# Performance work log

Hardware: AMD Instinct MI355X
Metric: run time of the kernel (lower is better)

Reference implementation:

```python
import jax, jax.numpy as jnp
import numpy as np
import math

N_HEAD = 16
HEAD_QKV = 1024  # total qkv width; head_dim = HEAD_QKV // N_HEAD
WM_DECAY_LENGTH = 2048
WM_DECAY_RATE = 1.0
WM_ECHOIC = 16


def decay_weight_matrix(n):
    # power_law decay, faithful to get_decay_weight_matrix
    dl = WM_DECAY_LENGTH - WM_ECHOIC + 1
    nums = jnp.linspace(0.0, 1.0, dl)
    decay_values = 1.0 - jnp.power(nums, 1.0 / (np.e * WM_DECAY_RATE))
    decay_values = jnp.concatenate([jnp.ones(WM_ECHOIC - 1), decay_values])  # [WM_DECAY_LENGTH]
    decay_values = decay_values[:n]
    idx = jnp.arange(n)[:, None] - jnp.arange(n)[None, :]  # [n,n], negative above diag
    mat = decay_values[jnp.clip(idx, 0, n - 1)]
    return jnp.tril(mat).astype(jnp.float32)


def setup_inputs() -> dict:
    key = jax.random.key(0)
    k1, k2, k3 = jax.random.split(key, 3)
    B, T, C = 2, 2048, 1024
    x = jax.random.normal(k1, (B, T, C), dtype=jnp.float32)
    W_attn = jax.random.normal(k2, (C, 3 * HEAD_QKV), dtype=jnp.float32) * (1.0 / math.sqrt(C))
    W_proj = jax.random.normal(k3, (HEAD_QKV, C), dtype=jnp.float32) * (1.0 / math.sqrt(HEAD_QKV))
    return {"x": x, "W_attn": W_attn, "W_proj": W_proj}


def reference(x, W_attn, W_proj):
    B, T, C = x.shape
    hd = HEAD_QKV // N_HEAD
    qkv = x @ W_attn  # [B,T,3*HEAD_QKV]
    q, k, v = jnp.split(qkv, 3, axis=-1)
    # [B,T,HQKV] -> [B,H,T,hd]
    q = q.reshape(B, T, N_HEAD, hd).transpose(0, 2, 1, 3)
    k = k.reshape(B, T, N_HEAD, hd).transpose(0, 2, 1, 3)
    v = v.reshape(B, T, N_HEAD, hd).transpose(0, 2, 1, 3)
    att = jnp.einsum('bhqd,bhkd->bhqk', q, k) * (1.0 / math.sqrt(hd))
    causal = jnp.tril(jnp.ones((T, T), dtype=bool))
    att = jnp.where(causal, att, -jnp.inf)
    att = jax.nn.softmax(att, axis=-1)
    att = att * decay_weight_matrix(T)  # post-softmax multiplicative decay
    y = jnp.einsum('bhqk,bhkd->bhqd', att, v)
    y = y.transpose(0, 2, 1, 3).reshape(B, T, HEAD_QKV)
    return y @ W_proj
```

## Files before the change

### kernel.cpp

```cpp
#include <hip/hip_runtime.h>
#include <math.h>

#define B_  2
#define T_  2048
#define C_  1024
#define NH_ 16
#define HD_ 64
#define N3_ 3072

typedef float f32x4 __attribute__((ext_vector_type(4)));
typedef short bf16x8 __attribute__((ext_vector_type(8)));
typedef unsigned short u16;
typedef float f32x4_base __attribute__((ext_vector_type(4)));
typedef f32x4_base __attribute__((aligned(4))) f32x4u;

#define QSCALE 0.18033688011112042f

#if __has_builtin(__builtin_amdgcn_exp2f)
#define EXP2(x) __builtin_amdgcn_exp2f(x)
#else
#define EXP2(x) exp2f(x)
#endif

__device__ __forceinline__ u16 f2bf(float x) {
  unsigned int u = __builtin_bit_cast(unsigned int, x);
  u += 0x7FFFu + ((u >> 16) & 1u);
  return (u16)(u >> 16);
}

__device__ __forceinline__ unsigned int cvt_pk_bf16(float lo, float hi) {
  unsigned int r;
  asm("v_cvt_pk_bf16_f32 %0, %1, %2" : "=v"(r) : "v"(lo), "v"(hi));
  return r;
}

#define GLD16(g, l) __builtin_amdgcn_global_load_lds( \
    (__attribute__((address_space(1))) void*)(g), \
    (__attribute__((address_space(3))) void*)(l), 16, 0, 0)

__global__ __launch_bounds__(256) void cvt4_kernel(const float* __restrict__ in,
                                                   u16* __restrict__ out, int n) {
  int i = (blockIdx.x * 256 + threadIdx.x) * 4;
  if (i >= n) return;
  float4 v = *(const float4*)(in + i);
  ushort4 o;
  o.x = f2bf(v.x); o.y = f2bf(v.y); o.z = f2bf(v.z); o.w = f2bf(v.w);
  *(ushort4*)(out + i) = o;
}

__global__ __launch_bounds__(256) void transpose_cvt_kernel(const float* __restrict__ in,
                                                            u16* __restrict__ out,
                                                            int R, int Cc) {
  __shared__ float tile[32][33];
  int c0 = blockIdx.x * 32, r0 = blockIdx.y * 32;
  int tx = threadIdx.x & 31, ty = threadIdx.x >> 5;
#pragma unroll
  for (int rr = ty; rr < 32; rr += 8)
    tile[rr][tx] = in[(size_t)(r0 + rr) * Cc + c0 + tx];
  __syncthreads();
#pragma unroll
  for (int rr = ty; rr < 32; rr += 8)
    out[(size_t)(c0 + rr) * R + r0 + tx] = f2bf(tile[tx][rr]);
}

__global__ __launch_bounds__(256) void decay_init_kernel(float* __restrict__ decR) {
  int j = blockIdx.x * 256 + threadIdx.x;
  if (j >= 2176) return;
  int d = 2047 - j;
  float v = 1.0f;
  if (d >= 15) v = 1.0f - powf((float)(d - 15) * (1.0f / 2032.0f), 0.36787944117144233f);
  decR[j] = v;
}

template<int MODE>
__global__ __launch_bounds__(256, 3) void gemm128_kernel(
    const u16* __restrict__ A, const u16* __restrict__ Bt,
    float* __restrict__ Cf, u16* __restrict__ Cq, u16* __restrict__ Vt,
    int M, int N, int K)
{
  __shared__ char lds[32768];
  const int lane = threadIdx.x & 63;
  const int wave = threadIdx.x >> 6;
  const int nxb = N >> 7;
  const int orig = blockIdx.x;
  const int cpx = (int)gridDim.x >> 3;
  const int wg = (orig & 7) * cpx + (orig >> 3);
  const int m0 = (wg / nxb) << 7;
  const int n0 = (wg % nxb) << 7;
  const int wm = wave >> 1, wn = wave & 1;

  f32x4 acc[4][4] = {};

#define GSTAGE(buf, k0)                                                          \
  {                                                                              \
    _Pragma("unroll")                                                            \
    for (int c = 0; c < 2; ++c) {                                                \
      int chunk = wave * 2048 + c * 1024;                                        \
      int row = (chunk >> 6) + (lane >> 2);                                      \
      int wb = ((lane & 3) << 4) ^ ((row & 3) << 4);                             \
      GLD16((const char*)(A  + (size_t)(m0 + row) * K + (k0)) + wb,              \
            lds + (buf) * 16384 + chunk);                                        \
      GLD16((const char*)(Bt + (size_t)(n0 + row) * K + (k0)) + wb,              \
            lds + (buf) * 16384 + 8192 + chunk);                                 \
    }                                                                            \
  }

  GSTAGE(0, 0);
  __syncthreads();

  for (int k0 = 0; k0 < K; k0 += 32) {
    const int cur = (k0 >> 5) & 1;
    if (k0 + 32 < K) GSTAGE(cur ^ 1, k0 + 32);
    const char* base = lds + cur * 16384;
    bf16x8 af[4], bfr[4];
#pragma unroll
    for (int m = 0; m < 4; ++m) {
      int row = wm * 64 + m * 16 + (lane & 15);
      int wb = ((lane >> 4) << 4) ^ ((row & 3) << 4);
      af[m] = *(const bf16x8*)(base + row * 64 + wb);
    }
#pragma unroll
    for (int n = 0; n < 4; ++n) {
      int row = wn * 64 + n * 16 + (lane & 15);
      int wb = ((lane >> 4) << 4) ^ ((row & 3) << 4);
      bfr[n] = *(const bf16x8*)(base + 8192 + row * 64 + wb);
    }
    __builtin_amdgcn_s_setprio(1);
#pragma unroll
    for (int m = 0; m < 4; ++m)
#pragma unroll
      for (int n = 0; n < 4; ++n)
        acc[m][n] = __builtin_amdgcn_mfma_f32_16x16x32_bf16(af[m], bfr[n], acc[m][n], 0, 0, 0);
    __builtin_amdgcn_s_setprio(0);
    __syncthreads();
  }

#pragma unroll
  for (int m = 0; m < 4; ++m) {
    int grow0 = m0 + wm * 64 + m * 16 + ((lane >> 4) << 2);
#pragma unroll
    for (int n = 0; n < 4; ++n) {
      int gcol = n0 + wn * 64 + n * 16 + (lane & 15);
      f32x4 v = acc[m][n];
      if (MODE == 0) {
        int bb = grow0 >> 11, tt0 = grow0 & 2047;
        int which = gcol >> 10, rem = gcol & 1023;
        int hh = rem >> 6, dd = rem & 63;
        if (which < 2) {
#pragma unroll
          for (int r = 0; r < 4; ++r) {
            float ov = (which == 0) ? v[r] * QSCALE : v[r];
            Cq[((size_t)(which * 32 + bb * 16 + hh) * 2048 + tt0 + r) * 64 + dd] = f2bf(ov);
          }
        } else {
          ushort4 o;
          o.x = f2bf(v[0]); o.y = f2bf(v[1]); o.z = f2bf(v[2]); o.w = f2bf(v[3]);
          *(ushort4*)(Vt + ((size_t)(bb * 16 + hh) * 64 + dd) * 2048 + tt0) = o;
        }
      } else {
#pragma unroll
        for (int r = 0; r < 4; ++r)
          Cf[(size_t)(grow0 + r) * N + gcol] = v[r];
      }
    }
  }
#undef GSTAGE
}

__global__ __launch_bounds__(256, 4) void attn_kernel(
    const u16* __restrict__ qkb, const u16* __restrict__ vtg,
    const float* __restrict__ decR, u16* __restrict__ yb)
{
  __shared__ char klds[2][8192];
  __shared__ char vlds[2][8192];
  __shared__ char plds[8192];

  const int lane = threadIdx.x & 63;
  const int wave = threadIdx.x >> 6;
  const int quad = lane >> 4;
  const int l15 = lane & 15;
  const int orig = blockIdx.x;
  const int sub = ((orig & 7) << 7) + (orig >> 3);
  const int a = sub & 7;
  const int bh = ((orig & 7) << 2) + ((sub >> 3) & 3);
  const int k4 = (sub >> 5) & 3;
  const int qt = k4 * 8 + ((k4 & 1) ? (7 - a) : a);
  const int b = bh >> 4, h = bh & 15;

  const u16* Q   = qkb + (size_t)bh * T_ * HD_;
  const u16* Kg  = qkb + (size_t)(32 + bh) * T_ * HD_;
  const u16* VTg = vtg + (size_t)bh * HD_ * T_;

  const int wrow = qt * 64 + wave * 16;
  const int q = wrow + l15;
  const int rbase0 = 2047 - q + quad * 4;
  const int prow = wave * 16 + l15;
  const int pswz = (l15 & 7) << 4;

  bf16x8 qa[2];
  { const u16* qp = Q + (size_t)q * HD_ + quad * 8;
    qa[0] = *(const bf16x8*)qp; qa[1] = *(const bf16x8*)(qp + 32); }

  f32x4 acc[4] = {};
  float lsum = 0.0f;

#define ASTAGE(buf, kt)                                                          \
  {                                                                              \
    _Pragma("unroll")                                                            \
    for (int c = 0; c < 2; ++c) {                                                \
      int chunk = wave * 2048 + c * 1024;                                        \
      int row = (chunk >> 7) + (lane >> 3);                                      \
      int wb = ((lane & 7) << 4) ^ ((row & 7) << 4);                             \
      GLD16((const char*)(Kg + (size_t)((kt) * 64 + row) * HD_) + wb,            \
            klds[buf] + chunk);                                                  \
      GLD16((const char*)(VTg + (size_t)row * T_ + (kt) * 64) + wb,              \
            vlds[buf] + chunk);                                                  \
    }                                                                            \
  }

  ASTAGE(0, 0);
  __syncthreads();

  const int nkt = qt + 1;
  for (int kt = 0; kt < nkt; ++kt) {
    const int cur = kt & 1;
    if (kt + 1 < nkt) ASTAGE(cur ^ 1, kt + 1);

    bf16x8 kf[4][2];
#pragma unroll
    for (int f = 0; f < 4; ++f) {
      int krow = f * 16 + l15;
      int base = krow * 128;
      int msk = (krow & 7) << 4;
      kf[f][0] = *(const bf16x8*)(klds[cur] + base + ((quad * 16) ^ msk));
      kf[f][1] = *(const bf16x8*)(klds[cur] + base + ((64 + quad * 16) ^ msk));
    }

    const float* dR = decR + (rbase0 + kt * 64);
    f32x4 dB[4];
#pragma unroll
    for (int f = 0; f < 4; ++f) dB[f] = *(const f32x4u*)(dR + f * 16);

    f32x4 s[4];
    __builtin_amdgcn_s_setprio(1);
#pragma unroll
    for (int f = 0; f < 4; ++f) {
      f32x4 t = {};
      t = __builtin_amdgcn_mfma_f32_16x16x32_bf16(kf[f][0], qa[0], t, 0, 0, 0);
      t = __builtin_amdgcn_mfma_f32_16x16x32_bf16(kf[f][1], qa[1], t, 0, 0, 0);
      s[f] = t;
    }
    __builtin_amdgcn_s_setprio(0);

    if (kt == qt) {
#pragma unroll
      for (int f = 0; f < 4; ++f) {
        int key0 = kt * 64 + f * 16 + quad * 4;
#pragma unroll
        for (int r = 0; r < 4; ++r)
          if (key0 + r > q) s[f][r] = -1e30f;
      }
    }

#pragma unroll
    for (int f = 0; f < 4; ++f) {
      f32x4 p;
#pragma unroll
      for (int r = 0; r < 4; ++r) p[r] = EXP2(s[f][r]);
      lsum += (p[0] + p[1]) + (p[2] + p[3]);
      unsigned int w0 = cvt_pk_bf16(p[0] * dB[f][0], p[1] * dB[f][1]);
      unsigned int w1 = cvt_pk_bf16(p[2] * dB[f][2], p[3] * dB[f][3]);
      uint2 wv; wv.x = w0; wv.y = w1;
      *(uint2*)(plds + prow * 128 + ((f * 32 + quad * 8) ^ pswz)) = wv;
    }

    bf16x8 vf[4][2];
#pragma unroll
    for (int n = 0; n < 4; ++n) {
      int vrow = n * 16 + l15;
      int mskv = (vrow & 7) << 4;
#pragma unroll
      for (int ks = 0; ks < 2; ++ks)
        vf[n][ks] = *(const bf16x8*)(vlds[cur] + vrow * 128 + ((ks * 64 + quad * 16) ^ mskv));
    }

    __builtin_amdgcn_s_setprio(1);
#pragma unroll
    for (int ks = 0; ks < 2; ++ks) {
      bf16x8 pa = *(const bf16x8*)(plds + prow * 128 + ((ks * 64 + quad * 16) ^ pswz));
#pragma unroll
      for (int n = 0; n < 4; ++n)
        acc[n] = __builtin_amdgcn_mfma_f32_16x16x32_bf16(pa, vf[n][ks], acc[n], 0, 0, 0);
    }
    __builtin_amdgcn_s_setprio(0);
    __syncthreads();
  }
#undef ASTAGE

  lsum += __shfl_xor(lsum, 16); lsum += __shfl_xor(lsum, 32);
  float rb[4];
#pragma unroll
  for (int r = 0; r < 4; ++r)
    rb[r] = 1.0f / __shfl(lsum, quad * 4 + r, 16);
#pragma unroll
  for (int n = 0; n < 4; ++n) {
    int d = h * 64 + n * 16 + l15;
#pragma unroll
    for (int r = 0; r < 4; ++r) {
      int t = wrow + quad * 4 + r;
      yb[((size_t)b * T_ + t) * 1024 + d] = f2bf(acc[n][r] * rb[r]);
    }
  }
}

extern "C" void kernel_launch(void* const* d_in, const int* in_sizes, int n_in,
                              void* d_out, int out_size, void* d_ws, size_t ws_size,
                              hipStream_t stream) {
  const float* x  = (const float*)d_in[0];
  const float* Wa = (const float*)d_in[1];
  const float* Wp = (const float*)d_in[2];
  float* out = (float*)d_out;
  char* ws = (char*)d_ws;

  u16*   xb    = (u16*)(ws + 0);
  u16*   WaT   = (u16*)(ws + 8388608);
  u16*   WpT   = (u16*)(ws + 14680064);
  u16*   qkb   = (u16*)(ws + 16777216);
  float* decR  = (float*)(ws + 33554432);
  u16*   VT    = (u16*)(ws + 41943040);
  u16*   yb    = xb;

  decay_init_kernel<<<9, 256, 0, stream>>>(decR);
  cvt4_kernel<<<4096, 256, 0, stream>>>(x, xb, B_ * T_ * C_);
  transpose_cvt_kernel<<<dim3(96, 32), 256, 0, stream>>>(Wa, WaT, C_, N3_);
  transpose_cvt_kernel<<<dim3(32, 32), 256, 0, stream>>>(Wp, WpT, C_, C_);

  gemm128_kernel<0><<<768, 256, 0, stream>>>(
      xb, WaT, nullptr, qkb, VT, B_ * T_, N3_, C_);
  attn_kernel<<<1024, 256, 0, stream>>>(qkb, VT, decR, yb);
  gemm128_kernel<1><<<256, 256, 0, stream>>>(
      yb, WpT, out, nullptr, nullptr, B_ * T_, 1024, 1024);
}
```

Baseline: 119.0 us.

## Process two 64-row query groups per attention block to reuse K/V tiles

Result: slower. 122.0 us (+2.6%).

```diff
diff --git a/kernel.cpp b/kernel.cpp
--- a/kernel.cpp
+++ b/kernel.cpp
@@ -167,42 +167,47 @@
 #undef GSTAGE
 }
 
-__global__ __launch_bounds__(256, 4) void attn_kernel(
+__global__ __launch_bounds__(256, 3) void attn_kernel(
     const u16* __restrict__ qkb, const u16* __restrict__ vtg,
     const float* __restrict__ decR, u16* __restrict__ yb)
 {
   __shared__ char klds[2][8192];
   __shared__ char vlds[2][8192];
-  __shared__ char plds[8192];
+  __shared__ u16 plds[128 * 72];
 
   const int lane = threadIdx.x & 63;
   const int wave = threadIdx.x >> 6;
   const int quad = lane >> 4;
   const int l15 = lane & 15;
   const int orig = blockIdx.x;
-  const int sub = ((orig & 7) << 7) + (orig >> 3);
-  const int a = sub & 7;
-  const int bh = ((orig & 7) << 2) + ((sub >> 3) & 3);
-  const int k4 = (sub >> 5) & 3;
-  const int qt = k4 * 8 + ((k4 & 1) ? (7 - a) : a);
+  const int xcd = orig & 7;
+  const int s6 = orig >> 3;
+  const int bh = (xcd << 2) + (s6 & 3);
+  const int tile = s6 >> 2;
+  const int qt = tile < 8 ? tile : 23 - tile;
   const int b = bh >> 4, h = bh & 15;
 
   const u16* Q   = qkb + (size_t)bh * T_ * HD_;
   const u16* Kg  = qkb + (size_t)(32 + bh) * T_ * HD_;
   const u16* VTg = vtg + (size_t)bh * HD_ * T_;
 
-  const int wrow = qt * 64 + wave * 16;
-  const int q = wrow + l15;
-  const int rbase0 = 2047 - q + quad * 4;
-  const int prow = wave * 16 + l15;
-  const int pswz = (l15 & 7) << 4;
-
-  bf16x8 qa[2];
-  { const u16* qp = Q + (size_t)q * HD_ + quad * 8;
-    qa[0] = *(const bf16x8*)qp; qa[1] = *(const bf16x8*)(qp + 32); }
-
-  f32x4 acc[4] = {};
-  float lsum = 0.0f;
+  const int wrow0 = qt * 128 + wave * 16;
+  const int q0 = wrow0 + l15;
+  const int q1 = q0 + 64;
+  const int rb0 = 2047 - q0 + quad * 4;
+  const int rb1 = rb0 - 64;
+  const int prow0 = wave * 16 + l15;
+
+  bf16x8 qa[2][2];
+#pragma unroll
+  for (int g = 0; g < 2; ++g) {
+    const u16* qp = Q + (size_t)(q0 + g * 64) * HD_ + quad * 8;
+    qa[g][0] = *(const bf16x8*)qp;
+    qa[g][1] = *(const bf16x8*)(qp + 32);
+  }
+
+  f32x4 acc[2][4] = {};
+  float lsum[2] = {0.0f, 0.0f};
 
 #define ASTAGE(buf, kt)                                                          \
   {                                                                              \
@@ -221,10 +226,11 @@
   ASTAGE(0, 0);
   __syncthreads();
 
-  const int nkt = qt + 1;
+  const int nkt = 2 * qt + 2;
   for (int kt = 0; kt < nkt; ++kt) {
     const int cur = kt & 1;
     if (kt + 1 < nkt) ASTAGE(cur ^ 1, kt + 1);
+    const bool act0 = (kt <= 2 * qt);
 
     bf16x8 kf[4][2];
 #pragma unroll
@@ -236,29 +242,52 @@
       kf[f][1] = *(const bf16x8*)(klds[cur] + base + ((64 + quad * 16) ^ msk));
     }
 
-    const float* dR = decR + (rbase0 + kt * 64);
-    f32x4 dB[4];
-#pragma unroll
-    for (int f = 0; f < 4; ++f) dB[f] = *(const f32x4u*)(dR + f * 16);
-
-    f32x4 s[4];
+    f32x4 d0[4], d1[4];
+    const float* dR1 = decR + (rb1 + kt * 64);
+#pragma unroll
+    for (int f = 0; f < 4; ++f) d1[f] = *(const f32x4u*)(dR1 + f * 16);
+    if (act0) {
+      const float* dR0 = decR + (rb0 + kt * 64);
+#pragma unroll
+      for (int f = 0; f < 4; ++f) d0[f] = *(const f32x4u*)(dR0 + f * 16);
+    }
+
+    f32x4 s0[4], s1[4];
     __builtin_amdgcn_s_setprio(1);
 #pragma unroll
     for (int f = 0; f < 4; ++f) {
       f32x4 t = {};
-      t = __builtin_amdgcn_mfma_f32_16x16x32_bf16(kf[f][0], qa[0], t, 0, 0, 0);
-      t = __builtin_amdgcn_mfma_f32_16x16x32_bf16(kf[f][1], qa[1], t, 0, 0, 0);
-      s[f] = t;
+      t = __builtin_amdgcn_mfma_f32_16x16x32_bf16(kf[f][0], qa[1][0], t, 0, 0, 0);
+      t = __builtin_amdgcn_mfma_f32_16x16x32_bf16(kf[f][1], qa[1][1], t, 0, 0, 0);
+      s1[f] = t;
+    }
+    if (act0) {
+#pragma unroll
+      for (int f = 0; f < 4; ++f) {
+        f32x4 t = {};
+        t = __builtin_amdgcn_mfma_f32_16x16x32_bf16(kf[f][0], qa[0][0], t, 0, 0, 0);
+        t = __builtin_amdgcn_mfma_f32_16x16x32_bf16(kf[f][1], qa[0][1], t, 0, 0, 0);
+        s0[f] = t;
+      }
     }
     __builtin_amdgcn_s_setprio(0);
 
-    if (kt == qt) {
+    if (kt == 2 * qt) {
 #pragma unroll
       for (int f = 0; f < 4; ++f) {
         int key0 = kt * 64 + f * 16 + quad * 4;
 #pragma unroll
         for (int r = 0; r < 4; ++r)
-          if (key0 + r > q) s[f][r] = -1e30f;
+          if (key0 + r > q0) s0[f][r] = -1e30f;
+      }
+    }
+    if (kt == 2 * qt + 1) {
+#pragma unroll
+      for (int f = 0; f < 4; ++f) {
+        int key0 = kt * 64 + f * 16 + quad * 4;
+#pragma unroll
+        for (int r = 0; r < 4; ++r)
+          if (key0 + r > q1) s1[f][r] = -1e30f;
       }
     }
 
@@ -266,12 +295,25 @@
     for (int f = 0; f < 4; ++f) {
       f32x4 p;
 #pragma unroll
-      for (int r = 0; r < 4; ++r) p[r] = EXP2(s[f][r]);
-      lsum += (p[0] + p[1]) + (p[2] + p[3]);
-      unsigned int w0 = cvt_pk_bf16(p[0] * dB[f][0], p[1] * dB[f][1]);
-      unsigned int w1 = cvt_pk_bf16(p[2] * dB[f][2], p[3] * dB[f][3]);
+      for (int r = 0; r < 4; ++r) p[r] = EXP2(s1[f][r]);
+      lsum[1] += (p[0] + p[1]) + (p[2] + p[3]);
+      unsigned int w0 = cvt_pk_bf16(p[0] * d1[f][0], p[1] * d1[f][1]);
+      unsigned int w1 = cvt_pk_bf16(p[2] * d1[f][2], p[3] * d1[f][3]);
       uint2 wv; wv.x = w0; wv.y = w1;
-      *(uint2*)(plds + prow * 128 + ((f * 32 + quad * 8) ^ pswz)) = wv;
+      *(uint2*)(plds + (size_t)(64 + prow0) * 72 + f * 16 + quad * 4) = wv;
+    }
+    if (act0) {
+#pragma unroll
+      for (int f = 0; f < 4; ++f) {
+        f32x4 p;
+#pragma unroll
+        for (int r = 0; r < 4; ++r) p[r] = EXP2(s0[f][r]);
+        lsum[0] += (p[0] + p[1]) + (p[2] + p[3]);
+        unsigned int w0 = cvt_pk_bf16(p[0] * d0[f][0], p[1] * d0[f][1]);
+        unsigned int w1 = cvt_pk_bf16(p[2] * d0[f][2], p[3] * d0[f][3]);
+        uint2 wv; wv.x = w0; wv.y = w1;
+        *(uint2*)(plds + (size_t)prow0 * 72 + f * 16 + quad * 4) = wv;
+      }
     }
 
     bf16x8 vf[4][2];
@@ -287,28 +329,42 @@
     __builtin_amdgcn_s_setprio(1);
 #pragma unroll
     for (int ks = 0; ks < 2; ++ks) {
-      bf16x8 pa = *(const bf16x8*)(plds + prow * 128 + ((ks * 64 + quad * 16) ^ pswz));
+      bf16x8 pa = *(const bf16x8*)(plds + (size_t)(64 + prow0) * 72 + ks * 32 + quad * 8);
 #pragma unroll
       for (int n = 0; n < 4; ++n)
-        acc[n] = __builtin_amdgcn_mfma_f32_16x16x32_bf16(pa, vf[n][ks], acc[n], 0, 0, 0);
+        acc[1][n] = __builtin_amdgcn_mfma_f32_16x16x32_bf16(pa, vf[n][ks], acc[1][n], 0, 0, 0);
+    }
+    if (act0) {
+#pragma unroll
+      for (int ks = 0; ks < 2; ++ks) {
+        bf16x8 pa = *(const bf16x8*)(plds + (size_t)prow0 * 72 + ks * 32 + quad * 8);
+#pragma unroll
+        for (int n = 0; n < 4; ++n)
+          acc[0][n] = __builtin_amdgcn_mfma_f32_16x16x32_bf16(pa, vf[n][ks], acc[0][n], 0, 0, 0);
+      }
     }
     __builtin_amdgcn_s_setprio(0);
     __syncthreads();
   }
 #undef ASTAGE
 
-  lsum += __shfl_xor(lsum, 16); lsum += __shfl_xor(lsum, 32);
-  float rb[4];
-#pragma unroll
-  for (int r = 0; r < 4; ++r)
-    rb[r] = 1.0f / __shfl(lsum, quad * 4 + r, 16);
-#pragma unroll
-  for (int n = 0; n < 4; ++n) {
-    int d = h * 64 + n * 16 + l15;
-#pragma unroll
-    for (int r = 0; r < 4; ++r) {
-      int t = wrow + quad * 4 + r;
-      yb[((size_t)b * T_ + t) * 1024 + d] = f2bf(acc[n][r] * rb[r]);
+#pragma unroll
+  for (int g = 0; g < 2; ++g) {
+    float lv = lsum[g];
+    lv += __shfl_xor(lv, 16);
+    lv += __shfl_xor(lv, 32);
+    float rb[4];
+#pragma unroll
+    for (int r = 0; r < 4; ++r)
+      rb[r] = 1.0f / __shfl(lv, quad * 4 + r, 16);
+#pragma unroll
+    for (int n = 0; n < 4; ++n) {
+      int d = h * 64 + n * 16 + l15;
+#pragma unroll
+      for (int r = 0; r < 4; ++r) {
+        int t = wrow0 + g * 64 + quad * 4 + r;
+        yb[((size_t)b * T_ + t) * 1024 + d] = f2bf(acc[g][n][r] * rb[r]);
+      }
     }
   }
 }
@@ -337,7 +393,7 @@
 
   gemm128_kernel<0><<<768, 256, 0, stream>>>(
       xb, WaT, nullptr, qkb, VT, B_ * T_, N3_, C_);
-  attn_kernel<<<1024, 256, 0, stream>>>(qkb, VT, decR, yb);
+  attn_kernel<<<512, 256, 0, stream>>>(qkb, VT, decR, yb);
   gemm128_kernel<1><<<256, 256, 0, stream>>>(
       yb, WpT, out, nullptr, nullptr, B_ * T_, 1024, 1024);
 }
```
